# Performance work log

Measured on AMD Instinct MI355X. Metric: run time of the kernel, lower is better.

## Reference

```python
import jax, jax.numpy as jnp
import numpy as np

# COCO-17 body parts (padded to max length with -1)
_PARTS = [[0,1,2,3,4],[5,6,11,12],[5,7,9],[6,8,10],[11,13,15],[12,14,16]]
_P = len(_PARTS)
_L = max(len(p) for p in _PARTS)
_IDX_NP = np.full((_P, _L), -1, dtype=np.int32)
for _p, _ix in enumerate(_PARTS):
    _IDX_NP[_p, :len(_ix)] = _ix
SAFE_IDX = jnp.asarray(np.clip(_IDX_NP, 0, None))   # (P,L)
VALID = jnp.asarray(_IDX_NP >= 0)                   # (P,L)
NUM_HEADS = 4
LN_EPS = 1e-5


def setup_inputs() -> dict:
    key = jax.random.key(0)
    ks = jax.random.split(key, 8)
    B, T, J, D = 32, 512, 17, 128
    s = 1.0 / np.sqrt(D)
    return {
        "h_joint": jax.random.normal(ks[0], (B, T, J, D), jnp.float32),
        "mask_joint": jax.random.uniform(ks[1], (B, T, J, 1), jnp.float32),
        "W_proj": jax.random.normal(ks[2], (D, D), jnp.float32) * s,
        "b_proj": jnp.zeros((D,), jnp.float32),
        "W_in": jax.random.normal(ks[3], (3 * D, D), jnp.float32) * s,
        "b_in": jnp.zeros((3 * D,), jnp.float32),
        "W_out": jax.random.normal(ks[4], (D, D), jnp.float32) * s,
        "b_out": jnp.zeros((D,), jnp.float32),
        "ln_g": jnp.ones((D,), jnp.float32),
        "ln_b": jnp.zeros((D,), jnp.float32),
    }


def reference(h_joint, mask_joint, W_proj, b_proj, W_in, b_in, W_out, b_out, ln_g, ln_b):
    B, T, J, D = h_joint.shape
    P, L = SAFE_IDX.shape
    H = NUM_HEADS
    dh = D // H

    # 1) gather joints per part + 2) mask-aware mean pool -> part tokens (B,T,P,D)
    m = mask_joint[..., 0] > 0.05                      # (B,T,J) bool
    hg = jnp.take(h_joint, SAFE_IDX, axis=2)           # (B,T,P,L,D)
    mg = jnp.take(m, SAFE_IDX, axis=2) & VALID         # (B,T,P,L)
    mf = mg.astype(h_joint.dtype)
    denom = jnp.clip(jnp.sum(mf, axis=3), 1e-6, None)  # (B,T,P)
    tok = jnp.einsum('btpld,btpl->btpd', hg, mf) / denom[..., None]

    tok = tok @ W_proj.T + b_proj                      # proj_in

    # 3) MHA across parts per frame (eval mode: dropout off)
    BT = B * T
    q = tok.reshape(BT, P, D)
    qkv = q @ W_in.T + b_in                            # (BT,P,3D)
    qh, kh, vh = (a.reshape(BT, P, H, dh).transpose(0, 2, 1, 3)
                  for a in jnp.split(qkv, 3, axis=-1))  # each (BT,H,P,dh)
    scores = jnp.einsum('bhqd,bhkd->bhqk', qh, kh) / np.sqrt(dh)
    w = jax.nn.softmax(scores, axis=-1)                # (BT,H,P,P)
    o = jnp.einsum('bhqk,bhkd->bhqd', w, vh)
    o = o.transpose(0, 2, 1, 3).reshape(BT, P, D) @ W_out.T + b_out

    # 4) residual + LayerNorm
    y = q + o
    mu = jnp.mean(y, axis=-1, keepdims=True)
    var = jnp.mean(jnp.square(y - mu), axis=-1, keepdims=True)
    y = (y - mu) * jax.lax.rsqrt(var + LN_EPS) * ln_g + ln_b

    part_out = y.reshape(B, T, P, D)
    attn_weights = jnp.mean(w, axis=1)                 # avg heads -> (BT,P,P)
    part_importance = jnp.mean(attn_weights, axis=1).reshape(B, T, P)
    return part_out, part_importance
```

## Files before the change

### kernel.cpp

```cpp
#include <hip/hip_runtime.h>
#include <hip/hip_bf16.h>

typedef __hip_bfloat16 bf16;
typedef __attribute__((ext_vector_type(8))) short short8v;
typedef __attribute__((ext_vector_type(4))) float f32x4;

#define NB   32
#define NTT  512
#define NJ   17
#define ND   128
#define NP   6
#define NH   4
#define NDH  32
#define NBT  (NB*NTT)
#define NG   4
#define NTOK (NG*NP)
#define NMT  2
#define NTHR 512
#define TSTR 136
#define YSTR 132

#define WS_WP 0
#define WS_WC 16384
#define WS_WO 65536

#define OFF_POOL 0
#define OFF_TOKP 6528
#define OFF_Q    13056
#define OFF_K    19584
#define OFF_V    26112
#define OFF_Y    19584
#define OFF_PROB 32640
#define OFF_MU   34944
#define OFF_INV  35040
#define ARENA_SZ 35136

__device__ __forceinline__ float bf2f(unsigned short u) {
    return __uint_as_float(((unsigned)u) << 16);
}
__device__ __forceinline__ f32x4 MFMA(short8v a, short8v b, f32x4 c) {
    return __builtin_amdgcn_mfma_f32_16x16x32_bf16(a, b, c, 0, 0, 0);
}
__device__ __forceinline__ short8v ldB(const bf16* __restrict__ W, int nt, int ks, int lane) {
    return *reinterpret_cast<const short8v*>(W + (nt*16 + (lane & 15))*ND + ks*32 + ((lane >> 4) << 3));
}
__device__ __forceinline__ short8v ldsA(const bf16* __restrict__ s, int mt, int ks, int lane) {
    int row = mt*16 + (lane & 15);
    if (row >= NTOK) row = NTOK - 1;
    return *reinterpret_cast<const short8v*>(s + row*TSTR + ks*32 + ((lane >> 4) << 3));
}

extern "C" __global__ __launch_bounds__(256)
void wconv(const float* __restrict__ Wp, const float* __restrict__ Wo,
           bf16* __restrict__ ws) {
    int i = blockIdx.x*256 + threadIdx.x;
    if (i < 16384) ws[WS_WP + i] = __float2bfloat16(Wp[i]);
    else           ws[WS_WO + (i - 16384)] = __float2bfloat16(Wo[i - 16384]);
}

extern "C" __global__ __launch_bounds__(128)
void wcomb(const float* __restrict__ Wp, const float* __restrict__ Wi,
           const float* __restrict__ bp, const float* __restrict__ bi,
           bf16* __restrict__ wc, float* __restrict__ bc) {
    __shared__ float s_red[128];
    const int n = blockIdx.x;
    const int k = threadIdx.x;
    float acc = 0.f;
    #pragma unroll 4
    for (int m = 0; m < 128; ++m)
        acc = fmaf(Wi[n*128+m], Wp[m*128+k], acc);
    wc[n*128+k] = __float2bfloat16(acc);
    s_red[k] = Wi[n*128+k]*bp[k];
    __syncthreads();
    #pragma unroll
    for (int s = 64; s > 0; s >>= 1) {
        if (k < s) s_red[k] += s_red[k+s];
        __syncthreads();
    }
    if (k == 0) bc[n] = s_red[0] + bi[n];
}

extern "C" __global__ __launch_bounds__(NTHR, 8)
void bpa_fused(const float* __restrict__ h_joint,
               const float* __restrict__ mask_joint,
               const bf16* __restrict__ wgt, const float* __restrict__ bc,
               const float* __restrict__ b_proj, const float* __restrict__ b_out,
               const float* __restrict__ ln_g,  const float* __restrict__ ln_b,
               float* __restrict__ out)
{
    __shared__ __align__(16) unsigned char s_arena[ARENA_SZ];
    bf16*  s_pool  = reinterpret_cast<bf16*>(s_arena + OFF_POOL);
    bf16*  s_tokp  = reinterpret_cast<bf16*>(s_arena + OFF_TOKP);
    bf16*  s_q     = reinterpret_cast<bf16*>(s_arena + OFF_Q);
    bf16*  s_k     = reinterpret_cast<bf16*>(s_arena + OFF_K);
    bf16*  s_v     = reinterpret_cast<bf16*>(s_arena + OFF_V);
    float* s_y     = reinterpret_cast<float*>(s_arena + OFF_Y);
    float* s_probs = reinterpret_cast<float*>(s_arena + OFF_PROB);
    float* s_mu    = reinterpret_cast<float*>(s_arena + OFF_MU);
    float* s_inv   = reinterpret_cast<float*>(s_arena + OFF_INV);

    const int tid  = threadIdx.x;
    const int lane = tid & 63;
    const int w    = tid >> 6;
    const long frame0 = (long)blockIdx.x * NG;

    short8v bwp[4];
    #pragma unroll
    for (int ks = 0; ks < 4; ++ks) bwp[ks] = ldB(wgt + WS_WP, w, ks, lane);

    {
        const int f = tid >> 7;
        const int d = tid & (ND-1);
        const float* hcol = h_joint + (frame0 + f)*(long)(NJ*ND) + d;
        const float* mrow = mask_joint + (frame0 + f)*(long)NJ;

        float hv[NJ];
        #pragma unroll
        for (int j = 0; j < NJ; ++j) hv[j] = hcol[j*ND];
        unsigned mb = 0;
        #pragma unroll
        for (int j = 0; j < NJ; ++j)
            mb |= (mrow[j] > 0.05f) ? (1u << j) : 0u;
        #pragma unroll
        for (int j = 0; j < NJ; ++j)
            hv[j] = (mb >> j & 1) ? hv[j] : 0.f;

        float acc[NP];
        acc[0] = ((hv[0]+hv[1]) + (hv[2]+hv[3])) + hv[4];
        acc[1] = (hv[5]+hv[6]) + (hv[11]+hv[12]);
        acc[2] = hv[5]+hv[7]+hv[9];
        acc[3] = hv[6]+hv[8]+hv[10];
        acc[4] = hv[11]+hv[13]+hv[15];
        acc[5] = hv[12]+hv[14]+hv[16];
        const unsigned pm[NP] = {0x1Fu, 0x1860u, 0x2A0u, 0x540u, 0xA800u, 0x15000u};
        #pragma unroll
        for (int p = 0; p < NP; ++p) {
            float cnt = (float)__popc(mb & pm[p]);
            s_pool[(f*NP+p)*TSTR + d] = __float2bfloat16(acc[p] / fmaxf(cnt, 1e-6f));
        }
    }
    __syncthreads();

    {
        f32x4 acc[NMT];
        acc[0] = (f32x4)(0.f); acc[1] = (f32x4)(0.f);
        #pragma unroll
        for (int ks = 0; ks < 4; ++ks)
            #pragma unroll
            for (int mt = 0; mt < NMT; ++mt)
                acc[mt] = MFMA(ldsA(s_pool, mt, ks, lane), bwp[ks], acc[mt]);
        int col = w*16 + (lane & 15);
        float bv = b_proj[col];
        #pragma unroll
        for (int mt = 0; mt < NMT; ++mt)
            #pragma unroll
            for (int j = 0; j < 4; ++j) {
                int row = mt*16 + ((lane >> 4) << 2) + j;
                if (row < NTOK)
                    s_tokp[row*TSTR + col] = __float2bfloat16(acc[mt][j] + bv);
            }
    }
    #pragma unroll
    for (int t = 0; t < 3; ++t) {
        int nt = t*8 + w;
        short8v bw[4];
        #pragma unroll
        for (int ks = 0; ks < 4; ++ks) bw[ks] = ldB(wgt + WS_WC, nt, ks, lane);
        f32x4 acc[NMT];
        acc[0] = (f32x4)(0.f); acc[1] = (f32x4)(0.f);
        #pragma unroll
        for (int ks = 0; ks < 4; ++ks)
            #pragma unroll
            for (int mt = 0; mt < NMT; ++mt)
                acc[mt] = MFMA(ldsA(s_pool, mt, ks, lane), bw[ks], acc[mt]);
        bf16* dst = (t == 0) ? s_q : (t == 1) ? s_k : s_v;
        int lcol = w*16 + (lane & 15);
        float bv = bc[nt*16 + (lane & 15)];
        #pragma unroll
        for (int mt = 0; mt < NMT; ++mt)
            #pragma unroll
            for (int j = 0; j < 4; ++j) {
                int row = mt*16 + ((lane >> 4) << 2) + j;
                if (row < NTOK)
                    dst[row*TSTR + lcol] = __float2bfloat16(acc[mt][j] + bv);
            }
    }
    __syncthreads();

    if (tid < NG*NH*NP) {
        int f   = tid / (NH*NP);
        int rem = tid - f*(NH*NP);
        int h   = rem / NP;
        int qi  = rem - h*NP;
        const bf16* qrow = s_q + (f*NP+qi)*TSTR + h*NDH;
        float sc[NP];
        float mx = -1e30f;
        #pragma unroll
        for (int pk = 0; pk < NP; ++pk) {
            const bf16* krow = s_k + (f*NP+pk)*TSTR + h*NDH;
            float s = 0.f;
            #pragma unroll
            for (int c = 0; c < NDH; c += 4) {
                ushort4 uq = *reinterpret_cast<const ushort4*>(qrow + c);
                ushort4 uk = *reinterpret_cast<const ushort4*>(krow + c);
                s += bf2f(uq.x)*bf2f(uk.x) + bf2f(uq.y)*bf2f(uk.y)
                   + bf2f(uq.z)*bf2f(uk.z) + bf2f(uq.w)*bf2f(uk.w);
            }
            sc[pk] = s * 0.17677669529663688f;
            mx = fmaxf(mx, sc[pk]);
        }
        float den = 0.f, e[NP];
        #pragma unroll
        for (int pk = 0; pk < NP; ++pk) { e[pk] = expf(sc[pk]-mx); den += e[pk]; }
        float inv = 1.f/den;
        #pragma unroll
        for (int pk = 0; pk < NP; ++pk)
            s_probs[((f*NH+h)*NP+qi)*NP + pk] = e[pk]*inv;
    }
    __syncthreads();

    if (tid < NG*NP) {
        int f = tid / NP, pk = tid - f*NP;
        float s = 0.f;
        #pragma unroll
        for (int h = 0; h < NH; ++h)
            #pragma unroll
            for (int q = 0; q < NP; ++q)
                s += s_probs[((f*NH+h)*NP+q)*NP + pk];
        out[(long)NBT*NP*ND + (frame0+f)*NP + pk] = s * (1.f/24.f);
    }
    #pragma unroll
    for (int i = 0; i < (NTOK*ND)/NTHR; ++i) {
        int idx = i*NTHR + tid;
        int token = idx >> 7;
        int d = idx & (ND-1);
        int f = token / NP, qi = token - f*NP;
        int h = d >> 5;
        const float* pr = s_probs + ((f*NH+h)*NP+qi)*NP;
        float s = 0.f;
        #pragma unroll
        for (int pk = 0; pk < NP; ++pk) {
            float v = bf2f(reinterpret_cast<const unsigned short*>(s_v)[(f*NP+pk)*TSTR + d]);
            s += pr[pk]*v;
        }
        s_q[token*TSTR + d] = __float2bfloat16(s);
    }
    __syncthreads();

    {
        short8v bo[4];
        #pragma unroll
        for (int ks = 0; ks < 4; ++ks) bo[ks] = ldB(wgt + WS_WO, w, ks, lane);
        f32x4 acc[NMT];
        acc[0] = (f32x4)(0.f); acc[1] = (f32x4)(0.f);
        #pragma unroll
        for (int ks = 0; ks < 4; ++ks)
            #pragma unroll
            for (int mt = 0; mt < NMT; ++mt)
                acc[mt] = MFMA(ldsA(s_q, mt, ks, lane), bo[ks], acc[mt]);
        int col = w*16 + (lane & 15);
        float bv = b_out[col];
        #pragma unroll
        for (int mt = 0; mt < NMT; ++mt)
            #pragma unroll
            for (int j = 0; j < 4; ++j) {
                int row = mt*16 + ((lane >> 4) << 2) + j;
                if (row < NTOK) {
                    float resid = bf2f(*reinterpret_cast<const unsigned short*>(&s_tokp[row*TSTR + col]));
                    s_y[row*YSTR + col] = acc[mt][j] + bv + resid;
                }
            }
    }
    __syncthreads();

    if (tid < NTOK*4) {
        int token = tid >> 2, sub = tid & 3;
        const float* row = s_y + token*YSTR + sub*NDH;
        float s = 0.f, s2 = 0.f;
        #pragma unroll
        for (int j = 0; j < NDH; j += 4) {
            float4 v = *reinterpret_cast<const float4*>(row + j);
            s  += v.x + v.y + v.z + v.w;
            s2 += v.x*v.x + v.y*v.y + v.z*v.z + v.w*v.w;
        }
        s  += __shfl_xor(s, 1);  s  += __shfl_xor(s, 2);
        s2 += __shfl_xor(s2, 1); s2 += __shfl_xor(s2, 2);
        float mean = s * (1.f/128.f);
        float var  = s2 * (1.f/128.f) - mean*mean;
        if (sub == 0) {
            s_mu[token]  = mean;
            s_inv[token] = rsqrtf(var + 1e-5f);
        }
    }
    __syncthreads();

    #pragma unroll
    for (int i = 0; i < 2; ++i) {
        int idx4 = i*NTHR + tid;
        if (idx4 < NTOK*(ND/4)) {
            int token = idx4 >> 5;
            int dj = (idx4 & 31) << 2;
            float mean = s_mu[token], inv = s_inv[token];
            float4 v = *reinterpret_cast<const float4*>(s_y + token*YSTR + dj);
            float4 g = *reinterpret_cast<const float4*>(ln_g + dj);
            float4 b = *reinterpret_cast<const float4*>(ln_b + dj);
            float4 r;
            r.x = (v.x-mean)*inv*g.x + b.x;
            r.y = (v.y-mean)*inv*g.y + b.y;
            r.z = (v.z-mean)*inv*g.z + b.z;
            r.w = (v.w-mean)*inv*g.w + b.w;
            *reinterpret_cast<float4*>(out + (frame0*NP + token)*(long)ND + dj) = r;
        }
    }
}

extern "C" void kernel_launch(void* const* d_in, const int* in_sizes, int n_in,
                              void* d_out, int out_size, void* d_ws, size_t ws_size,
                              hipStream_t stream) {
    const float* h_joint = (const float*)d_in[0];
    const float* mask    = (const float*)d_in[1];
    const float* W_proj  = (const float*)d_in[2];
    const float* b_proj  = (const float*)d_in[3];
    const float* W_in    = (const float*)d_in[4];
    const float* b_in    = (const float*)d_in[5];
    const float* W_out   = (const float*)d_in[6];
    const float* b_out   = (const float*)d_in[7];
    const float* ln_g    = (const float*)d_in[8];
    const float* ln_b    = (const float*)d_in[9];
    float* out = (float*)d_out;
    bf16*  wgt = (bf16*)d_ws;
    float* bc  = (float*)((char*)d_ws + 163840);

    hipLaunchKernelGGL(wconv, dim3(32768/256), dim3(256), 0, stream,
                       W_proj, W_out, wgt);
    hipLaunchKernelGGL(wcomb, dim3(384), dim3(128), 0, stream,
                       W_proj, W_in, b_proj, b_in, wgt + WS_WC, bc);
    hipLaunchKernelGGL(bpa_fused, dim3(NBT/NG), dim3(NTHR), 0, stream,
                       h_joint, mask, wgt, bc, b_proj, b_out, ln_g, ln_b, out);
}
```

Baseline: 112.1 us.

## Make fused kernel persistent with register double-buffered h_joint prefetch

The main kernel now runs as a persistent grid of 1024 blocks, each looping over several 4-frame groups. Each iteration prefetches the next group's h_joint column and mask bits into a second register buffer so global loads overlap the MFMA, attention and LayerNorm stages. A new mconv kernel packs the mask into per-frame bitmasks beforehand, and __syncthreads is replaced by a barrier that waits only on LDS counters. This adds register pressure (occupancy hint lowered to 6) and one extra small launch, and reduces the number of blocks available to hide latency.

```diff
diff --git a/kernel.cpp b/kernel.cpp
--- a/kernel.cpp
+++ b/kernel.cpp
@@ -17,12 +17,16 @@
 #define NTOK (NG*NP)
 #define NMT  2
 #define NTHR 512
+#define GRID 1024
+#define NITER ((NBT/NG)/GRID)
 #define TSTR 136
 #define YSTR 132
 
 #define WS_WP 0
 #define WS_WC 16384
 #define WS_WO 65536
+#define WS_BC 163840
+#define WS_MB 165376
 
 #define OFF_POOL 0
 #define OFF_TOKP 6528
@@ -48,6 +52,11 @@
     int row = mt*16 + (lane & 15);
     if (row >= NTOK) row = NTOK - 1;
     return *reinterpret_cast<const short8v*>(s + row*TSTR + ks*32 + ((lane >> 4) << 3));
+}
+__device__ __forceinline__ void bsync() {
+    asm volatile("s_waitcnt lgkmcnt(0)" ::: "memory");
+    __builtin_amdgcn_s_barrier();
+    asm volatile("" ::: "memory");
 }
 
 extern "C" __global__ __launch_bounds__(256)
@@ -80,10 +89,21 @@
     if (k == 0) bc[n] = s_red[0] + bi[n];
 }
 
-extern "C" __global__ __launch_bounds__(NTHR, 8)
+extern "C" __global__ __launch_bounds__(256)
+void mconv(const float* __restrict__ mask, unsigned* __restrict__ mb) {
+    int fr = blockIdx.x*256 + threadIdx.x;
+    const float* m = mask + (long)fr*NJ;
+    unsigned b = 0;
+    #pragma unroll
+    for (int j = 0; j < NJ; ++j)
+        b |= (m[j] > 0.05f) ? (1u << j) : 0u;
+    mb[fr] = b;
+}
+
+extern "C" __global__ __launch_bounds__(NTHR, 6)
 void bpa_fused(const float* __restrict__ h_joint,
-               const float* __restrict__ mask_joint,
                const bf16* __restrict__ wgt, const float* __restrict__ bc,
+               const unsigned* __restrict__ mbuf,
                const float* __restrict__ b_proj, const float* __restrict__ b_out,
                const float* __restrict__ ln_g,  const float* __restrict__ ln_b,
                float* __restrict__ out)
@@ -102,215 +122,228 @@
     const int tid  = threadIdx.x;
     const int lane = tid & 63;
     const int w    = tid >> 6;
-    const long frame0 = (long)blockIdx.x * NG;
-
-    short8v bwp[4];
+    const int f    = tid >> 7;
+    const int d    = tid & (ND-1);
+
+    const long fr0   = (long)blockIdx.x * NG + f;
+    const float* hb0 = h_joint + fr0*(long)(NJ*ND) + d;
+    const long FSTEP = (long)GRID*NG;
+    const long HSTEP = FSTEP*(long)(NJ*ND);
+
+    float    hv[2][NJ];
+    unsigned mbv[2];
     #pragma unroll
-    for (int ks = 0; ks < 4; ++ks) bwp[ks] = ldB(wgt + WS_WP, w, ks, lane);
-
-    {
-        const int f = tid >> 7;
-        const int d = tid & (ND-1);
-        const float* hcol = h_joint + (frame0 + f)*(long)(NJ*ND) + d;
-        const float* mrow = mask_joint + (frame0 + f)*(long)NJ;
-
-        float hv[NJ];
+    for (int j = 0; j < NJ; ++j) hv[0][j] = hb0[j*ND];
+    mbv[0] = mbuf[fr0];
+
+    #pragma unroll
+    for (int it = 0; it < NITER; ++it) {
+        const long frame0 = (long)blockIdx.x*NG + (long)it*FSTEP;
+        const int  cur = it & 1, nxt = (it + 1) & 1;
+
+        {
+            unsigned mb = mbv[cur];
+            float t[NJ];
+            #pragma unroll
+            for (int j = 0; j < NJ; ++j)
+                t[j] = (mb >> j & 1) ? hv[cur][j] : 0.f;
+            float acc[NP];
+            acc[0] = ((t[0]+t[1]) + (t[2]+t[3])) + t[4];
+            acc[1] = (t[5]+t[6]) + (t[11]+t[12]);
+            acc[2] = t[5]+t[7]+t[9];
+            acc[3] = t[6]+t[8]+t[10];
+            acc[4] = t[11]+t[13]+t[15];
+            acc[5] = t[12]+t[14]+t[16];
+            const unsigned pm[NP] = {0x1Fu, 0x1860u, 0x2A0u, 0x540u, 0xA800u, 0x15000u};
+            #pragma unroll
+            for (int p = 0; p < NP; ++p) {
+                float cnt = (float)__popc(mb & pm[p]);
+                s_pool[(f*NP+p)*TSTR + d] = __float2bfloat16(acc[p] / fmaxf(cnt, 1e-6f));
+            }
+        }
+        if (it + 1 < NITER) {
+            const float* hn = hb0 + (long)(it+1)*HSTEP;
+            #pragma unroll
+            for (int j = 0; j < NJ; ++j) hv[nxt][j] = hn[j*ND];
+            mbv[nxt] = mbuf[fr0 + (long)(it+1)*FSTEP];
+        }
+        bsync();
+
+        {
+            short8v bwp[4];
+            #pragma unroll
+            for (int ks = 0; ks < 4; ++ks) bwp[ks] = ldB(wgt + WS_WP, w, ks, lane);
+            f32x4 acc[NMT];
+            acc[0] = (f32x4)(0.f); acc[1] = (f32x4)(0.f);
+            #pragma unroll
+            for (int ks = 0; ks < 4; ++ks)
+                #pragma unroll
+                for (int mt = 0; mt < NMT; ++mt)
+                    acc[mt] = MFMA(ldsA(s_pool, mt, ks, lane), bwp[ks], acc[mt]);
+            int col = w*16 + (lane & 15);
+            float bv = b_proj[col];
+            #pragma unroll
+            for (int mt = 0; mt < NMT; ++mt)
+                #pragma unroll
+                for (int j = 0; j < 4; ++j) {
+                    int row = mt*16 + ((lane >> 4) << 2) + j;
+                    if (row < NTOK)
+                        s_tokp[row*TSTR + col] = __float2bfloat16(acc[mt][j] + bv);
+                }
+        }
         #pragma unroll
-        for (int j = 0; j < NJ; ++j) hv[j] = hcol[j*ND];
-        unsigned mb = 0;
+        for (int t = 0; t < 3; ++t) {
+            int nt = t*8 + w;
+            short8v bw[4];
+            #pragma unroll
+            for (int ks = 0; ks < 4; ++ks) bw[ks] = ldB(wgt + WS_WC, nt, ks, lane);
+            f32x4 acc[NMT];
+            acc[0] = (f32x4)(0.f); acc[1] = (f32x4)(0.f);
+            #pragma unroll
+            for (int ks = 0; ks < 4; ++ks)
+                #pragma unroll
+                for (int mt = 0; mt < NMT; ++mt)
+                    acc[mt] = MFMA(ldsA(s_pool, mt, ks, lane), bw[ks], acc[mt]);
+            bf16* dst = (t == 0) ? s_q : (t == 1) ? s_k : s_v;
+            int lcol = w*16 + (lane & 15);
+            float bv = bc[nt*16 + (lane & 15)];
+            #pragma unroll
+            for (int mt = 0; mt < NMT; ++mt)
+                #pragma unroll
+                for (int j = 0; j < 4; ++j) {
+                    int row = mt*16 + ((lane >> 4) << 2) + j;
+                    if (row < NTOK)
+                        dst[row*TSTR + lcol] = __float2bfloat16(acc[mt][j] + bv);
+                }
+        }
+        bsync();
+
+        if (tid < NG*NH*NP) {
+            int ff  = tid / (NH*NP);
+            int rem = tid - ff*(NH*NP);
+            int h   = rem / NP;
+            int qi  = rem - h*NP;
+            const bf16* qrow = s_q + (ff*NP+qi)*TSTR + h*NDH;
+            float sc[NP];
+            float mx = -1e30f;
+            #pragma unroll
+            for (int pk = 0; pk < NP; ++pk) {
+                const bf16* krow = s_k + (ff*NP+pk)*TSTR + h*NDH;
+                float s = 0.f;
+                #pragma unroll
+                for (int c = 0; c < NDH; c += 4) {
+                    ushort4 uq = *reinterpret_cast<const ushort4*>(qrow + c);
+                    ushort4 uk = *reinterpret_cast<const ushort4*>(krow + c);
+                    s += bf2f(uq.x)*bf2f(uk.x) + bf2f(uq.y)*bf2f(uk.y)
+                       + bf2f(uq.z)*bf2f(uk.z) + bf2f(uq.w)*bf2f(uk.w);
+                }
+                sc[pk] = s * 0.17677669529663688f;
+                mx = fmaxf(mx, sc[pk]);
+            }
+            float den = 0.f, e[NP];
+            #pragma unroll
+            for (int pk = 0; pk < NP; ++pk) { e[pk] = expf(sc[pk]-mx); den += e[pk]; }
+            float inv = 1.f/den;
+            #pragma unroll
+            for (int pk = 0; pk < NP; ++pk)
+                s_probs[((ff*NH+h)*NP+qi)*NP + pk] = e[pk]*inv;
+        }
+        bsync();
+
+        if (tid < NG*NP) {
+            int ff = tid / NP, pk = tid - ff*NP;
+            float s = 0.f;
+            #pragma unroll
+            for (int h = 0; h < NH; ++h)
+                #pragma unroll
+                for (int q = 0; q < NP; ++q)
+                    s += s_probs[((ff*NH+h)*NP+q)*NP + pk];
+            out[(long)NBT*NP*ND + (frame0+ff)*NP + pk] = s * (1.f/24.f);
+        }
         #pragma unroll
-        for (int j = 0; j < NJ; ++j)
-            mb |= (mrow[j] > 0.05f) ? (1u << j) : 0u;
+        for (int i = 0; i < (NTOK*ND)/NTHR; ++i) {
+            int idx = i*NTHR + tid;
+            int token = idx >> 7;
+            int dd = idx & (ND-1);
+            int ff = token / NP, qi = token - ff*NP;
+            int h = dd >> 5;
+            const float* pr = s_probs + ((ff*NH+h)*NP+qi)*NP;
+            float s = 0.f;
+            #pragma unroll
+            for (int pk = 0; pk < NP; ++pk) {
+                float v = bf2f(reinterpret_cast<const unsigned short*>(s_v)[(ff*NP+pk)*TSTR + dd]);
+                s += pr[pk]*v;
+            }
+            s_q[token*TSTR + dd] = __float2bfloat16(s);
+        }
+        bsync();
+
+        {
+            short8v bo[4];
+            #pragma unroll
+            for (int ks = 0; ks < 4; ++ks) bo[ks] = ldB(wgt + WS_WO, w, ks, lane);
+            f32x4 acc[NMT];
+            acc[0] = (f32x4)(0.f); acc[1] = (f32x4)(0.f);
+            #pragma unroll
+            for (int ks = 0; ks < 4; ++ks)
+                #pragma unroll
+                for (int mt = 0; mt < NMT; ++mt)
+                    acc[mt] = MFMA(ldsA(s_q, mt, ks, lane), bo[ks], acc[mt]);
+            int col = w*16 + (lane & 15);
+            float bv = b_out[col];
+            #pragma unroll
+            for (int mt = 0; mt < NMT; ++mt)
+                #pragma unroll
+                for (int j = 0; j < 4; ++j) {
+                    int row = mt*16 + ((lane >> 4) << 2) + j;
+                    if (row < NTOK) {
+                        float resid = bf2f(*reinterpret_cast<const unsigned short*>(&s_tokp[row*TSTR + col]));
+                        s_y[row*YSTR + col] = acc[mt][j] + bv + resid;
+                    }
+                }
+        }
+        bsync();
+
+        if (tid < NTOK*4) {
+            int token = tid >> 2, sub = tid & 3;
+            const float* row = s_y + token*YSTR + sub*NDH;
+            float s = 0.f, s2 = 0.f;
+            #pragma unroll
+            for (int j = 0; j < NDH; j += 4) {
+                float4 v = *reinterpret_cast<const float4*>(row + j);
+                s  += v.x + v.y + v.z + v.w;
+                s2 += v.x*v.x + v.y*v.y + v.z*v.z + v.w*v.w;
+            }
+            s  += __shfl_xor(s, 1);  s  += __shfl_xor(s, 2);
+            s2 += __shfl_xor(s2, 1); s2 += __shfl_xor(s2, 2);
+            float mean = s * (1.f/128.f);
+            float var  = s2 * (1.f/128.f) - mean*mean;
+            if (sub == 0) {
+                s_mu[token]  = mean;
+                s_inv[token] = rsqrtf(var + 1e-5f);
+            }
+        }
+        bsync();
+
         #pragma unroll
-        for (int j = 0; j < NJ; ++j)
-            hv[j] = (mb >> j & 1) ? hv[j] : 0.f;
-
-        float acc[NP];
-        acc[0] = ((hv[0]+hv[1]) + (hv[2]+hv[3])) + hv[4];
-        acc[1] = (hv[5]+hv[6]) + (hv[11]+hv[12]);
-        acc[2] = hv[5]+hv[7]+hv[9];
-        acc[3] = hv[6]+hv[8]+hv[10];
-        acc[4] = hv[11]+hv[13]+hv[15];
-        acc[5] = hv[12]+hv[14]+hv[16];
-        const unsigned pm[NP] = {0x1Fu, 0x1860u, 0x2A0u, 0x540u, 0xA800u, 0x15000u};
-        #pragma unroll
-        for (int p = 0; p < NP; ++p) {
-            float cnt = (float)__popc(mb & pm[p]);
-            s_pool[(f*NP+p)*TSTR + d] = __float2bfloat16(acc[p] / fmaxf(cnt, 1e-6f));
-        }
-    }
-    __syncthreads();
-
-    {
-        f32x4 acc[NMT];
-        acc[0] = (f32x4)(0.f); acc[1] = (f32x4)(0.f);
-        #pragma unroll
-        for (int ks = 0; ks < 4; ++ks)
-            #pragma unroll
-            for (int mt = 0; mt < NMT; ++mt)
-                acc[mt] = MFMA(ldsA(s_pool, mt, ks, lane), bwp[ks], acc[mt]);
-        int col = w*16 + (lane & 15);
-        float bv = b_proj[col];
-        #pragma unroll
-        for (int mt = 0; mt < NMT; ++mt)
-            #pragma unroll
-            for (int j = 0; j < 4; ++j) {
-                int row = mt*16 + ((lane >> 4) << 2) + j;
-                if (row < NTOK)
-                    s_tokp[row*TSTR + col] = __float2bfloat16(acc[mt][j] + bv);
-            }
-    }
-    #pragma unroll
-    for (int t = 0; t < 3; ++t) {
-        int nt = t*8 + w;
-        short8v bw[4];
-        #pragma unroll
-        for (int ks = 0; ks < 4; ++ks) bw[ks] = ldB(wgt + WS_WC, nt, ks, lane);
-        f32x4 acc[NMT];
-        acc[0] = (f32x4)(0.f); acc[1] = (f32x4)(0.f);
-        #pragma unroll
-        for (int ks = 0; ks < 4; ++ks)
-            #pragma unroll
-            for (int mt = 0; mt < NMT; ++mt)
-                acc[mt] = MFMA(ldsA(s_pool, mt, ks, lane), bw[ks], acc[mt]);
-        bf16* dst = (t == 0) ? s_q : (t == 1) ? s_k : s_v;
-        int lcol = w*16 + (lane & 15);
-        float bv = bc[nt*16 + (lane & 15)];
-        #pragma unroll
-        for (int mt = 0; mt < NMT; ++mt)
-            #pragma unroll
-            for (int j = 0; j < 4; ++j) {
-                int row = mt*16 + ((lane >> 4) << 2) + j;
-                if (row < NTOK)
-                    dst[row*TSTR + lcol] = __float2bfloat16(acc[mt][j] + bv);
-            }
-    }
-    __syncthreads();
-
-    if (tid < NG*NH*NP) {
-        int f   = tid / (NH*NP);
-        int rem = tid - f*(NH*NP);
-        int h   = rem / NP;
-        int qi  = rem - h*NP;
-        const bf16* qrow = s_q + (f*NP+qi)*TSTR + h*NDH;
-        float sc[NP];
-        float mx = -1e30f;
-        #pragma unroll
-        for (int pk = 0; pk < NP; ++pk) {
-            const bf16* krow = s_k + (f*NP+pk)*TSTR + h*NDH;
-            float s = 0.f;
-            #pragma unroll
-            for (int c = 0; c < NDH; c += 4) {
-                ushort4 uq = *reinterpret_cast<const ushort4*>(qrow + c);
-                ushort4 uk = *reinterpret_cast<const ushort4*>(krow + c);
-                s += bf2f(uq.x)*bf2f(uk.x) + bf2f(uq.y)*bf2f(uk.y)
-                   + bf2f(uq.z)*bf2f(uk.z) + bf2f(uq.w)*bf2f(uk.w);
-            }
-            sc[pk] = s * 0.17677669529663688f;
-            mx = fmaxf(mx, sc[pk]);
-        }
-        float den = 0.f, e[NP];
-        #pragma unroll
-        for (int pk = 0; pk < NP; ++pk) { e[pk] = expf(sc[pk]-mx); den += e[pk]; }
-        float inv = 1.f/den;
-        #pragma unroll
-        for (int pk = 0; pk < NP; ++pk)
-            s_probs[((f*NH+h)*NP+qi)*NP + pk] = e[pk]*inv;
-    }
-    __syncthreads();
-
-    if (tid < NG*NP) {
-        int f = tid / NP, pk = tid - f*NP;
-        float s = 0.f;
-        #pragma unroll
-        for (int h = 0; h < NH; ++h)
-            #pragma unroll
-            for (int q = 0; q < NP; ++q)
-                s += s_probs[((f*NH+h)*NP+q)*NP + pk];
-        out[(long)NBT*NP*ND + (frame0+f)*NP + pk] = s * (1.f/24.f);
-    }
-    #pragma unroll
-    for (int i = 0; i < (NTOK*ND)/NTHR; ++i) {
-        int idx = i*NTHR + tid;
-        int token = idx >> 7;
-        int d = idx & (ND-1);
-        int f = token / NP, qi = token - f*NP;
-        int h = d >> 5;
-        const float* pr = s_probs + ((f*NH+h)*NP+qi)*NP;
-        float s = 0.f;
-        #pragma unroll
-        for (int pk = 0; pk < NP; ++pk) {
-            float v = bf2f(reinterpret_cast<const unsigned short*>(s_v)[(f*NP+pk)*TSTR + d]);
-            s += pr[pk]*v;
-        }
-        s_q[token*TSTR + d] = __float2bfloat16(s);
-    }
-    __syncthreads();
-
-    {
-        short8v bo[4];
-        #pragma unroll
-        for (int ks = 0; ks < 4; ++ks) bo[ks] = ldB(wgt + WS_WO, w, ks, lane);
-        f32x4 acc[NMT];
-        acc[0] = (f32x4)(0.f); acc[1] = (f32x4)(0.f);
-        #pragma unroll
-        for (int ks = 0; ks < 4; ++ks)
-            #pragma unroll
-            for (int mt = 0; mt < NMT; ++mt)
-                acc[mt] = MFMA(ldsA(s_q, mt, ks, lane), bo[ks], acc[mt]);
-        int col = w*16 + (lane & 15);
-        float bv = b_out[col];
-        #pragma unroll
-        for (int mt = 0; mt < NMT; ++mt)
-            #pragma unroll
-            for (int j = 0; j < 4; ++j) {
-                int row = mt*16 + ((lane >> 4) << 2) + j;
-                if (row < NTOK) {
-                    float resid = bf2f(*reinterpret_cast<const unsigned short*>(&s_tokp[row*TSTR + col]));
-                    s_y[row*YSTR + col] = acc[mt][j] + bv + resid;
-                }
-            }
-    }
-    __syncthreads();
-
-    if (tid < NTOK*4) {
-        int token = tid >> 2, sub = tid & 3;
-        const float* row = s_y + token*YSTR + sub*NDH;
-        float s = 0.f, s2 = 0.f;
-        #pragma unroll
-        for (int j = 0; j < NDH; j += 4) {
-            float4 v = *reinterpret_cast<const float4*>(row + j);
-            s  += v.x + v.y + v.z + v.w;
-            s2 += v.x*v.x + v.y*v.y + v.z*v.z + v.w*v.w;
-        }
-        s  += __shfl_xor(s, 1);  s  += __shfl_xor(s, 2);
-        s2 += __shfl_xor(s2, 1); s2 += __shfl_xor(s2, 2);
-        float mean = s * (1.f/128.f);
-        float var  = s2 * (1.f/128.f) - mean*mean;
-        if (sub == 0) {
-            s_mu[token]  = mean;
-            s_inv[token] = rsqrtf(var + 1e-5f);
-        }
-    }
-    __syncthreads();
-
-    #pragma unroll
-    for (int i = 0; i < 2; ++i) {
-        int idx4 = i*NTHR + tid;
-        if (idx4 < NTOK*(ND/4)) {
-            int token = idx4 >> 5;
-            int dj = (idx4 & 31) << 2;
-            float mean = s_mu[token], inv = s_inv[token];
-            float4 v = *reinterpret_cast<const float4*>(s_y + token*YSTR + dj);
-            float4 g = *reinterpret_cast<const float4*>(ln_g + dj);
-            float4 b = *reinterpret_cast<const float4*>(ln_b + dj);
-            float4 r;
-            r.x = (v.x-mean)*inv*g.x + b.x;
-            r.y = (v.y-mean)*inv*g.y + b.y;
-            r.z = (v.z-mean)*inv*g.z + b.z;
-            r.w = (v.w-mean)*inv*g.w + b.w;
-            *reinterpret_cast<float4*>(out + (frame0*NP + token)*(long)ND + dj) = r;
-        }
+        for (int i = 0; i < 2; ++i) {
+            int idx4 = i*NTHR + tid;
+            if (idx4 < NTOK*(ND/4)) {
+                int token = idx4 >> 5;
+                int dj = (idx4 & 31) << 2;
+                float mean = s_mu[token], inv = s_inv[token];
+                float4 v = *reinterpret_cast<const float4*>(s_y + token*YSTR + dj);
+                float4 g = *reinterpret_cast<const float4*>(ln_g + dj);
+                float4 b = *reinterpret_cast<const float4*>(ln_b + dj);
+                float4 r;
+                r.x = (v.x-mean)*inv*g.x + b.x;
+                r.y = (v.y-mean)*inv*g.y + b.y;
+                r.z = (v.z-mean)*inv*g.z + b.z;
+                r.w = (v.w-mean)*inv*g.w + b.w;
+                *reinterpret_cast<float4*>(out + (frame0*NP + token)*(long)ND + dj) = r;
+            }
+        }
+        bsync();
     }
 }
 
@@ -328,13 +361,16 @@
     const float* ln_g    = (const float*)d_in[8];
     const float* ln_b    = (const float*)d_in[9];
     float* out = (float*)d_out;
-    bf16*  wgt = (bf16*)d_ws;
-    float* bc  = (float*)((char*)d_ws + 163840);
+    bf16*     wgt  = (bf16*)d_ws;
+    float*    bc   = (float*)((char*)d_ws + WS_BC);
+    unsigned* mbuf = (unsigned*)((char*)d_ws + WS_MB);
 
     hipLaunchKernelGGL(wconv, dim3(32768/256), dim3(256), 0, stream,
                        W_proj, W_out, wgt);
     hipLaunchKernelGGL(wcomb, dim3(384), dim3(128), 0, stream,
                        W_proj, W_in, b_proj, b_in, wgt + WS_WC, bc);
-    hipLaunchKernelGGL(bpa_fused, dim3(NBT/NG), dim3(NTHR), 0, stream,
-                       h_joint, mask, wgt, bc, b_proj, b_out, ln_g, ln_b, out);
-}
+    hipLaunchKernelGGL(mconv, dim3(NBT/256), dim3(256), 0, stream,
+                       mask, mbuf);
+    hipLaunchKernelGGL(bpa_fused, dim3(GRID), dim3(NTHR), 0, stream,
+                       h_joint, wgt, bc, mbuf, b_proj, b_out, ln_g, ln_b, out);
+}
```

Result: slower. 287.4 us (+156.3%).
